# Performance work log

Hardware: AMD Instinct MI355X
Metric: run time of the kernel (lower is better)

The kernel has to match this reference:

```python
import jax, jax.numpy as jnp
import numpy as np

B, S, D = 2, 2048, 1024
N_HEADS = 16
PAT_HEADS = N_HEADS // 4          # MultiheadAttention num_heads = 4
HEAD_DIM = D // PAT_HEADS         # 256
SPARSITY_RATIO = 0.1
MEMORY_PRESSURE = 0.5
NEG_INF = -1e9


def setup_inputs() -> dict:
    key = jax.random.key(0)
    ks = jax.random.split(key, 16)
    sd = 1.0 / np.sqrt(D)
    sh = 1.0 / np.sqrt(D // 4)
    inp = {
        "q": jax.random.normal(ks[0], (B, S, D), jnp.float32),
        "k": jax.random.normal(ks[1], (B, S, D), jnp.float32),
        "v": jax.random.normal(ks[2], (B, S, D), jnp.float32),
        # sparsity predictor: Linear(D, D//4) -> ReLU -> Linear(D//4, 1) -> Sigmoid
        "w1": jax.random.uniform(ks[3], (D, D // 4), jnp.float32, -sd, sd),
        "b1": jax.random.uniform(ks[4], (D // 4,), jnp.float32, -sd, sd),
        "w2": jax.random.uniform(ks[5], (D // 4, 1), jnp.float32, -sh, sh),
        "b2": jax.random.uniform(ks[6], (1,), jnp.float32, -sh, sh),
        # MultiheadAttention in_proj (split) + out_proj, stored [in, out]
        "wq": jax.random.uniform(ks[7], (D, D), jnp.float32, -sd, sd),
        "bq": jnp.zeros((D,), jnp.float32),
        "wk": jax.random.uniform(ks[8], (D, D), jnp.float32, -sd, sd),
        "bk": jnp.zeros((D,), jnp.float32),
        "wv": jax.random.uniform(ks[9], (D, D), jnp.float32, -sd, sd),
        "bv": jnp.zeros((D,), jnp.float32),
        "wo": jax.random.uniform(ks[10], (D, D), jnp.float32, -sd, sd),
        "bo": jnp.zeros((D,), jnp.float32),
    }
    return inp


def reference(q, k, v, w1, b1, w2, b2, wq, bq, wk, bk, wv, bv, wo, bo):
    # learned importance scores -> boolean mask of active tokens
    h = jax.nn.relu(q @ w1 + b1)                       # [B,S,D//4]
    scores = jax.nn.sigmoid(h @ w2 + b2)[..., 0]       # [B,S]
    threshold = SPARSITY_RATIO * (1.0 + MEMORY_PRESSURE)
    mask = scores > threshold                          # [B,S] bool

    # original module flattens all active tokens across batch into ONE
    # sequence and runs MHA over that subset; we express the identical math
    # with a fixed-shape masked attention over the flattened [B*S] tokens.
    N = B * S
    mf = mask.reshape(N)                               # [N]
    qf = q.reshape(N, D)
    kf = k.reshape(N, D)
    vf = v.reshape(N, D)

    qp = (qf @ wq + bq).reshape(N, PAT_HEADS, HEAD_DIM)
    kp = (kf @ wk + bk).reshape(N, PAT_HEADS, HEAD_DIM)
    vp = (vf @ wv + bv).reshape(N, PAT_HEADS, HEAD_DIM)

    scale = 1.0 / np.sqrt(HEAD_DIM)
    logits = jnp.einsum("nhd,mhd->hnm", qp * scale, kp)   # [H,N,N]
    logits = jnp.where(mf[None, None, :], logits, NEG_INF)  # only active keys
    attn = jax.nn.softmax(logits, axis=-1)
    ctx = jnp.einsum("hnm,mhd->nhd", attn, vp).reshape(N, D)
    out = ctx @ wo + bo                                 # [N,D]

    # scatter back: inactive query positions stay zero
    out = jnp.where(mf[:, None], out, 0.0)
    return out.reshape(B, S, D)
```

## Files before the change

kernel.cpp:

```cpp
#include <hip/hip_runtime.h>
#include <hip/hip_bf16.h>
#include <math.h>

typedef __bf16 bf16x8 __attribute__((ext_vector_type(8)));
typedef __bf16 bf16x4 __attribute__((ext_vector_type(4)));
typedef float  f32x4  __attribute__((ext_vector_type(4)));
typedef short  s16x8  __attribute__((ext_vector_type(8)));

#define N_TOK  4096
#define DMODEL 1024
#define NHEAD  4
#define DHEAD  256

__device__ __forceinline__ f32x4 mfma16x16(bf16x8 a, bf16x8 b, f32x4 c) {
    return __builtin_amdgcn_mfma_f32_16x16x32_bf16(a, b, c, 0, 0, 0);
}

__device__ __forceinline__ void gload_lds16(const void* gsrc, void* ldst) {
    __builtin_amdgcn_global_load_lds(
        (const __attribute__((address_space(1))) void*)gsrc,
        (__attribute__((address_space(3))) void*)ldst, 16, 0, 0);
}

#define G_LDT 72

template<typename OutT, bool AF32>
__global__ __launch_bounds__(256, 2)
void gemm_mixed(const void* __restrict__ Av, int lda,
                const float* __restrict__ B, int ldb,
                const float* __restrict__ bias,
                OutT* __restrict__ C, int ldc,
                float scale, int relu, const float* __restrict__ rowmask)
{
    __shared__ __align__(16) short As[64 * G_LDT];
    __shared__ __align__(16) short Bs[128 * G_LDT];
    const int tid  = threadIdx.x;
    const int lane = tid & 63;
    const int wv   = tid >> 6;
    const int c16  = lane & 15;
    const int quad = lane >> 4;
    const int m0 = blockIdx.x * 64;
    const int n0 = blockIdx.y * 128;

    f32x4 acc[4][2];
    #pragma unroll
    for (int i = 0; i < 4; ++i)
        #pragma unroll
        for (int j = 0; j < 2; ++j)
            acc[i][j] = (f32x4){0.f, 0.f, 0.f, 0.f};

    const int bn = tid & 127;
    const int bh = tid >> 7;

    for (int k0 = 0; k0 < 1024; k0 += 64) {
        if (AF32) {
            const float* A = (const float*)Av;
            #pragma unroll
            for (int r = 0; r < 4; ++r) {
                int i = tid + r * 256;
                int m = i >> 4, c = i & 15;
                f32x4 t = *(const f32x4*)(A + (size_t)(m0 + m) * lda + k0 + c * 4);
                bf16x4 b;
                #pragma unroll
                for (int j = 0; j < 4; ++j) b[j] = (__bf16)t[j];
                *(bf16x4*)(&As[m * G_LDT + c * 4]) = b;
            }
        } else {
            const __bf16* A = (const __bf16*)Av;
            #pragma unroll
            for (int r = 0; r < 2; ++r) {
                int i = tid + r * 256;
                int m = i >> 3, c = i & 7;
                *(s16x8*)(&As[m * G_LDT + c * 8]) =
                    *(const s16x8*)(A + (size_t)(m0 + m) * lda + k0 + c * 8);
            }
        }
        {
            const float* bp = B + (size_t)(k0 + bh * 32) * ldb + n0 + bn;
            #pragma unroll
            for (int g = 0; g < 4; ++g) {
                bf16x8 t;
                #pragma unroll
                for (int j = 0; j < 8; ++j) t[j] = (__bf16)bp[(size_t)(g * 8 + j) * ldb];
                *(bf16x8*)(&Bs[bn * G_LDT + bh * 32 + g * 8]) = t;
            }
        }
        __syncthreads();
        #pragma unroll
        for (int ks = 0; ks < 2; ++ks) {
            bf16x8 af[4], bfr[2];
            #pragma unroll
            for (int t = 0; t < 4; ++t)
                af[t] = *(const bf16x8*)(&As[(t * 16 + c16) * G_LDT + ks * 32 + quad * 8]);
            #pragma unroll
            for (int t = 0; t < 2; ++t)
                bfr[t] = *(const bf16x8*)(&Bs[(wv * 32 + t * 16 + c16) * G_LDT + ks * 32 + quad * 8]);
            #pragma unroll
            for (int tm = 0; tm < 4; ++tm)
                #pragma unroll
                for (int tn = 0; tn < 2; ++tn)
                    acc[tm][tn] = mfma16x16(af[tm], bfr[tn], acc[tm][tn]);
        }
        __syncthreads();
    }

    #pragma unroll
    for (int tm = 0; tm < 4; ++tm) {
        #pragma unroll
        for (int r = 0; r < 4; ++r) {
            int row = m0 + tm * 16 + quad * 4 + r;
            float mk = rowmask ? rowmask[row] : 1.0f;
            #pragma unroll
            for (int tn = 0; tn < 2; ++tn) {
                int col = n0 + wv * 32 + tn * 16 + c16;
                float val = (acc[tm][tn][r] + bias[col]) * scale;
                if (relu) val = fmaxf(val, 0.0f);
                val *= mk;
                C[(size_t)row * ldc + col] = (OutT)val;
            }
        }
    }
}

__global__ void score_mask_kernel(const __bf16* __restrict__ h,
                                  const float* __restrict__ w2,
                                  const float* __restrict__ b2,
                                  float* __restrict__ maskf)
{
    int lane = threadIdx.x & 63;
    int tok  = blockIdx.x * 4 + (threadIdx.x >> 6);
    const __bf16* hr = h + (size_t)tok * 256;
    float s = 0.f;
    #pragma unroll
    for (int j = 0; j < 4; ++j) {
        int c = j * 64 + lane;
        s += (float)hr[c] * w2[c];
    }
    #pragma unroll
    for (int o = 1; o < 64; o <<= 1) s += __shfl_xor(s, o);
    if (lane == 0) {
        float x = s + b2[0];
        maskf[tok] = (x > -1.7346010553881064f) ? 1.0f : 0.0f;
    }
}

__global__ __launch_bounds__(256)
void transpose_kernel(const __bf16* __restrict__ in, __bf16* __restrict__ out)
{
    __shared__ __align__(16) short tile[64 * 72];
    const int tid = threadIdx.x;
    const int t0 = blockIdx.x * 64;
    const int c0 = blockIdx.y * 64;
    #pragma unroll
    for (int it = 0; it < 2; ++it) {
        int i = tid + it * 256;
        int tok = i >> 3, ch = i & 7;
        s16x8 v = *(const s16x8*)((const short*)in + (size_t)(t0 + tok) * DMODEL + c0 + ch * 8);
        #pragma unroll
        for (int j = 0; j < 8; ++j)
            tile[(ch * 8 + j) * 72 + tok] = v[j];
    }
    __syncthreads();
    #pragma unroll
    for (int it = 0; it < 2; ++it) {
        int i = tid + it * 256;
        int col = i >> 3, och = i & 7;
        s16x8 v = *(const s16x8*)(&tile[col * 72 + och * 8]);
        *(s16x8*)((short*)out + (size_t)(c0 + col) * N_TOK + t0 + och * 8) = v;
    }
}

template<bool SPLIT>
__global__ __launch_bounds__(256, 2)
void attn_kernel(const __bf16* __restrict__ qp, const __bf16* __restrict__ kp,
                 const __bf16* __restrict__ vpT, const float* __restrict__ maskf,
                 __bf16* __restrict__ O0, __bf16* __restrict__ O1,
                 float* __restrict__ lbuf)
{
    __shared__ __align__(16) short Ks[64 * 256];
    __shared__ __align__(16) short Vs[256 * 64];
    __shared__ __align__(16) short PsA[4 * 16 * 64];

    const int tid  = threadIdx.x;
    const int lane = tid & 63;
    const int wv   = tid >> 6;
    const int c16  = lane & 15;
    const int quad = lane >> 4;
    const int swz  = c16 & 7;
    const int head = blockIdx.y;
    const int ksp  = SPLIT ? blockIdx.z : 0;
    const int kbase = ksp * (SPLIT ? 2048 : 0);
    const int kend  = kbase + (SPLIT ? 2048 : 4096);
    const int q0   = blockIdx.x * 64 + wv * 16;
    short* Ps = PsA + wv * 16 * 64;
    __bf16* Ob = (SPLIT && ksp == 1) ? O1 : O0;

    bf16x8 qf[8];
    #pragma unroll
    for (int c = 0; c < 8; ++c)
        qf[c] = *(const bf16x8*)(qp + (size_t)(q0 + c16) * DMODEL + head * DHEAD + c * 32 + quad * 8);

    f32x4 o[16];
    #pragma unroll
    for (int t = 0; t < 16; ++t) o[t] = (f32x4){0.f, 0.f, 0.f, 0.f};
    float psum[4] = {0.f, 0.f, 0.f, 0.f};

    const int kRow0 = wv * 16 + (lane >> 5);
    const int kCh   = lane & 31;
    const int vRow0 = wv * 64 + (lane >> 3);
    const int vCh   = (lane & 7) ^ ((lane >> 3) & 7);

    #pragma unroll 1
    for (int n0 = kbase; n0 < kend; n0 += 64) {
        #pragma unroll
        for (int g = 0; g < 8; ++g) {
            int key = kRow0 + g * 2;
            int c   = kCh ^ (key & 7);
            const char* src = (const char*)(kp + (size_t)(n0 + key) * DMODEL + head * DHEAD) + c * 16;
            gload_lds16(src, (char*)Ks + (wv * 16 + g * 2) * 512);
        }
        #pragma unroll
        for (int g = 0; g < 8; ++g) {
            int row = vRow0 + g * 8;
            const char* src = (const char*)(vpT + (size_t)(head * DHEAD + row) * N_TOK + n0) + vCh * 16;
            gload_lds16(src, (char*)Vs + (wv * 64 + g * 8) * 128);
        }
        __syncthreads();

        f32x4 s[4];
        #pragma unroll
        for (int kt = 0; kt < 4; ++kt) s[kt] = (f32x4){0.f, 0.f, 0.f, 0.f};
        __builtin_amdgcn_s_setprio(1);
        #pragma unroll
        for (int c = 0; c < 8; ++c)
            #pragma unroll
            for (int kt = 0; kt < 4; ++kt) {
                bf16x8 bfr = *(const bf16x8*)(&Ks[(kt * 16 + c16) * 256 + (((c * 4 + quad) ^ swz) << 3)]);
                s[kt] = mfma16x16(qf[c], bfr, s[kt]);
            }
        __builtin_amdgcn_s_setprio(0);

        #pragma unroll
        for (int kt = 0; kt < 4; ++kt) {
            float biasv = (maskf[n0 + kt * 16 + c16] - 1.0f) * 1e9f;
            #pragma unroll
            for (int r = 0; r < 4; ++r) {
                float p = __expf(s[kt][r] + biasv);
                psum[r] += p;
                int qrow = quad * 4 + r;
                int ch = (kt * 2 + (c16 >> 3)) ^ (qrow & 7);
                *(__bf16*)&Ps[qrow * 64 + ch * 8 + swz] = (__bf16)p;
            }
        }

        __builtin_amdgcn_s_waitcnt(0xc07f);

        __builtin_amdgcn_s_setprio(1);
        #pragma unroll
        for (int kstep = 0; kstep < 2; ++kstep) {
            bf16x8 pf = *(const bf16x8*)(&Ps[c16 * 64 + (((kstep * 4 + quad) ^ swz) << 3)]);
            #pragma unroll
            for (int t = 0; t < 16; ++t) {
                bf16x8 vf = *(const bf16x8*)(&Vs[(t * 16 + c16) * 64 + (((kstep * 4 + quad) ^ swz) << 3)]);
                o[t] = mfma16x16(pf, vf, o[t]);
            }
        }
        __builtin_amdgcn_s_setprio(0);
        __syncthreads();
    }

    float inv[4];
    #pragma unroll
    for (int r = 0; r < 4; ++r) {
        float t = psum[r];
        t += __shfl_xor(t, 1);
        t += __shfl_xor(t, 2);
        t += __shfl_xor(t, 4);
        t += __shfl_xor(t, 8);
        if (SPLIT && c16 == 0)
            lbuf[(size_t)(ksp * NHEAD + head) * N_TOK + q0 + quad * 4 + r] = t;
        inv[r] = 1.0f / t;
    }
    #pragma unroll
    for (int t = 0; t < 16; ++t)
        #pragma unroll
        for (int r = 0; r < 4; ++r) {
            float val = o[t][r] * inv[r];
            Ob[(size_t)(q0 + quad * 4 + r) * DMODEL + head * DHEAD + t * 16 + c16] = (__bf16)val;
        }
}

__global__ void combine_kernel(const __bf16* __restrict__ O0,
                               const __bf16* __restrict__ O1,
                               const float* __restrict__ lbuf,
                               __bf16* __restrict__ out)
{
    int idx  = blockIdx.x * 256 + threadIdx.x;
    int tok  = idx >> 7;
    int g    = idx & 127;
    int head = g >> 5;
    float a = lbuf[(size_t)head * N_TOK + tok];
    float b = lbuf[(size_t)(NHEAD + head) * N_TOK + tok];
    float w0 = a / (a + b);
    float w1 = 1.0f - w0;
    size_t off = (size_t)tok * DMODEL + g * 8;
    bf16x8 x = *(const bf16x8*)(O0 + off);
    bf16x8 y = *(const bf16x8*)(O1 + off);
    bf16x8 z;
    #pragma unroll
    for (int j = 0; j < 8; ++j) z[j] = (__bf16)(w0 * (float)x[j] + w1 * (float)y[j]);
    *(bf16x8*)(out + off) = z;
}

extern "C" void kernel_launch(void* const* d_in, const int* in_sizes, int n_in,
                              void* d_out, int out_size, void* d_ws, size_t ws_size,
                              hipStream_t stream)
{
    (void)in_sizes; (void)n_in; (void)out_size;
    const float* q  = (const float*)d_in[0];
    const float* k  = (const float*)d_in[1];
    const float* v  = (const float*)d_in[2];
    const float* w1 = (const float*)d_in[3];
    const float* b1 = (const float*)d_in[4];
    const float* w2 = (const float*)d_in[5];
    const float* b2 = (const float*)d_in[6];
    const float* wq = (const float*)d_in[7];
    const float* bq = (const float*)d_in[8];
    const float* wk = (const float*)d_in[9];
    const float* bk = (const float*)d_in[10];
    const float* wvw = (const float*)d_in[11];
    const float* bv = (const float*)d_in[12];
    const float* wo = (const float*)d_in[13];
    const float* bo = (const float*)d_in[14];

    if (ws_size < 35667968u) return;

    char* ws = (char*)d_ws;
    float*  maskf = (float*)ws;
    __bf16* hbuf  = (__bf16*)(ws + 16384);
    __bf16* qp    = (__bf16*)(ws + 16384 + 2097152);
    __bf16* kpb   = qp  + 4194304;
    __bf16* vpb   = kpb + 4194304;
    __bf16* ctx   = vpb + 4194304;
    __bf16* O1    = (__bf16*)(ws + 35667968u);
    float*  lbuf  = (float*)(ws + 35667968u + 8388608u);
    const bool split = ws_size >= 35667968u + 8388608u + 131072u;

    __bf16* vpT = (__bf16*)d_out;

    gemm_mixed<__bf16, true><<<dim3(64, 2), 256, 0, stream>>>(q, 1024, w1, 256, b1, hbuf, 256, 1.0f, 1, nullptr);
    score_mask_kernel<<<1024, 256, 0, stream>>>(hbuf, w2, b2, maskf);
    gemm_mixed<__bf16, true><<<dim3(64, 8), 256, 0, stream>>>(q, 1024, wq, 1024, bq, qp, 1024, 0.0625f, 0, nullptr);
    gemm_mixed<__bf16, true><<<dim3(64, 8), 256, 0, stream>>>(k, 1024, wk, 1024, bk, kpb, 1024, 1.0f, 0, nullptr);
    gemm_mixed<__bf16, true><<<dim3(64, 8), 256, 0, stream>>>(v, 1024, wvw, 1024, bv, vpb, 1024, 1.0f, 0, nullptr);
    transpose_kernel<<<dim3(64, 16), 256, 0, stream>>>(vpb, vpT);

    if (split) {
        attn_kernel<true><<<dim3(64, 4, 2), 256, 0, stream>>>(qp, kpb, vpT, maskf, ctx, O1, lbuf);
        combine_kernel<<<2048, 256, 0, stream>>>(ctx, O1, lbuf, ctx);
    } else {
        attn_kernel<false><<<dim3(64, 4, 1), 256, 0, stream>>>(qp, kpb, vpT, maskf, ctx, nullptr, nullptr);
    }

    gemm_mixed<float, false><<<dim3(64, 8), 256, 0, stream>>>(ctx, 1024, wo, 1024, bo, (float*)d_out, 1024, 1.0f, 0, maskf);
}
```

Baseline: 359.0 us.

## Pre-transpose weights to bf16 and compute V projection directly transposed

Adds a weight transpose-and-convert kernel so every GEMM reads a K-contiguous bf16 B operand instead of doing strided per-element fp32 loads of the weights. The GEMM is reworked to a 128x64 tile with an XOR-swizzled LDS layout, uses direct global-to-LDS loads for bf16 operands, and raises wave priority around the MFMA section. The V projection is computed as wvT·vᵀ with a per-row bias, which writes V already transposed and removes the separate activation transpose kernel. It costs five extra transpose launches per call and reuses the output and hbuf buffers as scratch for the transposed weights.

```diff
diff --git a/kernel.cpp b/kernel.cpp
--- a/kernel.cpp
+++ b/kernel.cpp
@@ -22,25 +22,53 @@
         (__attribute__((address_space(3))) void*)ldst, 16, 0, 0);
 }
 
-#define G_LDT 72
-
-template<typename OutT, bool AF32>
+__global__ __launch_bounds__(256)
+void transposew_kernel(const float* __restrict__ in, __bf16* __restrict__ out,
+                       int R, int C)
+{
+    __shared__ __align__(16) __bf16 tile[64 * 72];
+    const int tid = threadIdx.x;
+    const int r0 = blockIdx.x * 64;
+    const int c0 = blockIdx.y * 64;
+    #pragma unroll
+    for (int it = 0; it < 4; ++it) {
+        int i = tid + it * 256;
+        int row = i >> 4, c4 = i & 15;
+        f32x4 v = *(const f32x4*)(in + (size_t)(r0 + row) * C + c0 + c4 * 4);
+        #pragma unroll
+        for (int j = 0; j < 4; ++j)
+            tile[(c4 * 4 + j) * 72 + row] = (__bf16)v[j];
+    }
+    __syncthreads();
+    #pragma unroll
+    for (int it = 0; it < 2; ++it) {
+        int i = tid + it * 256;
+        int col = i >> 3, ch = i & 7;
+        s16x8 v = *(const s16x8*)(&tile[col * 72 + ch * 8]);
+        *(s16x8*)((short*)out + (size_t)(c0 + col) * R + r0 + ch * 8) = v;
+    }
+}
+
+template<typename OutT, bool AF32, bool BF32, bool BIASROW>
 __global__ __launch_bounds__(256, 2)
-void gemm_mixed(const void* __restrict__ Av, int lda,
-                const float* __restrict__ B, int ldb,
-                const float* __restrict__ bias,
-                OutT* __restrict__ C, int ldc,
-                float scale, int relu, const float* __restrict__ rowmask)
-{
-    __shared__ __align__(16) short As[64 * G_LDT];
-    __shared__ __align__(16) short Bs[128 * G_LDT];
+void gemm_bt(const void* __restrict__ Av, int lda,
+             const void* __restrict__ Bv, int ldb,
+             const float* __restrict__ bias,
+             OutT* __restrict__ C, int ldc,
+             float scale, int relu, const float* __restrict__ rowmask, int K)
+{
+    __shared__ __align__(16) short As[128 * 64];
+    __shared__ __align__(16) short Bs[64 * 64];
     const int tid  = threadIdx.x;
     const int lane = tid & 63;
     const int wv   = tid >> 6;
     const int c16  = lane & 15;
     const int quad = lane >> 4;
-    const int m0 = blockIdx.x * 64;
-    const int n0 = blockIdx.y * 128;
+    const int swz  = c16 & 7;
+    const int wr   = wv >> 1;
+    const int wc   = wv & 1;
+    const int m0 = blockIdx.x * 128;
+    const int n0 = blockIdx.y * 64;
 
     f32x4 acc[4][2];
     #pragma unroll
@@ -49,71 +77,92 @@
         for (int j = 0; j < 2; ++j)
             acc[i][j] = (f32x4){0.f, 0.f, 0.f, 0.f};
 
-    const int bn = tid & 127;
-    const int bh = tid >> 7;
-
-    for (int k0 = 0; k0 < 1024; k0 += 64) {
+    const int sRow = lane >> 3;
+    const int sCh  = (lane & 7) ^ (sRow & 7);
+
+    #pragma unroll 1
+    for (int k0 = 0; k0 < K; k0 += 64) {
         if (AF32) {
             const float* A = (const float*)Av;
             #pragma unroll
             for (int r = 0; r < 4; ++r) {
-                int i = tid + r * 256;
-                int m = i >> 4, c = i & 15;
-                f32x4 t = *(const f32x4*)(A + (size_t)(m0 + m) * lda + k0 + c * 4);
-                bf16x4 b;
+                int idx = tid + r * 256;
+                int row = idx >> 3, ch = idx & 7;
+                const float* ap = A + (size_t)(m0 + row) * lda + k0 + ch * 8;
+                f32x4 t0 = *(const f32x4*)ap;
+                f32x4 t1 = *(const f32x4*)(ap + 4);
+                bf16x8 b;
                 #pragma unroll
-                for (int j = 0; j < 4; ++j) b[j] = (__bf16)t[j];
-                *(bf16x4*)(&As[m * G_LDT + c * 4]) = b;
+                for (int j = 0; j < 4; ++j) { b[j] = (__bf16)t0[j]; b[j + 4] = (__bf16)t1[j]; }
+                *(bf16x8*)((char*)As + row * 128 + ((ch ^ (row & 7)) * 16)) = b;
             }
         } else {
             const __bf16* A = (const __bf16*)Av;
             #pragma unroll
+            for (int g = 0; g < 4; ++g) {
+                int row = 32 * wv + 8 * g + sRow;
+                const char* src = (const char*)(A + (size_t)(m0 + row) * lda + k0) + sCh * 16;
+                gload_lds16(src, (char*)As + (32 * wv + 8 * g) * 128);
+            }
+        }
+        if (BF32) {
+            const float* B = (const float*)Bv;
+            #pragma unroll
             for (int r = 0; r < 2; ++r) {
-                int i = tid + r * 256;
-                int m = i >> 3, c = i & 7;
-                *(s16x8*)(&As[m * G_LDT + c * 8]) =
-                    *(const s16x8*)(A + (size_t)(m0 + m) * lda + k0 + c * 8);
-            }
-        }
-        {
-            const float* bp = B + (size_t)(k0 + bh * 32) * ldb + n0 + bn;
-            #pragma unroll
-            for (int g = 0; g < 4; ++g) {
-                bf16x8 t;
+                int idx = tid + r * 256;
+                int row = idx >> 3, ch = idx & 7;
+                const float* bp = B + (size_t)(n0 + row) * ldb + k0 + ch * 8;
+                f32x4 t0 = *(const f32x4*)bp;
+                f32x4 t1 = *(const f32x4*)(bp + 4);
+                bf16x8 b;
                 #pragma unroll
-                for (int j = 0; j < 8; ++j) t[j] = (__bf16)bp[(size_t)(g * 8 + j) * ldb];
-                *(bf16x8*)(&Bs[bn * G_LDT + bh * 32 + g * 8]) = t;
+                for (int j = 0; j < 4; ++j) { b[j] = (__bf16)t0[j]; b[j + 4] = (__bf16)t1[j]; }
+                *(bf16x8*)((char*)Bs + row * 128 + ((ch ^ (row & 7)) * 16)) = b;
+            }
+        } else {
+            const __bf16* B = (const __bf16*)Bv;
+            #pragma unroll
+            for (int g = 0; g < 2; ++g) {
+                int row = 16 * wv + 8 * g + sRow;
+                const char* src = (const char*)(B + (size_t)(n0 + row) * ldb + k0) + sCh * 16;
+                gload_lds16(src, (char*)Bs + (16 * wv + 8 * g) * 128);
             }
         }
         __syncthreads();
+
+        __builtin_amdgcn_s_setprio(1);
         #pragma unroll
         for (int ks = 0; ks < 2; ++ks) {
             bf16x8 af[4], bfr[2];
+            int slot = ((ks * 4 + quad) ^ swz) * 16;
             #pragma unroll
             for (int t = 0; t < 4; ++t)
-                af[t] = *(const bf16x8*)(&As[(t * 16 + c16) * G_LDT + ks * 32 + quad * 8]);
+                af[t] = *(const bf16x8*)((char*)As + (wr * 64 + t * 16 + c16) * 128 + slot);
             #pragma unroll
             for (int t = 0; t < 2; ++t)
-                bfr[t] = *(const bf16x8*)(&Bs[(wv * 32 + t * 16 + c16) * G_LDT + ks * 32 + quad * 8]);
+                bfr[t] = *(const bf16x8*)((char*)Bs + (wc * 32 + t * 16 + c16) * 128 + slot);
             #pragma unroll
             for (int tm = 0; tm < 4; ++tm)
                 #pragma unroll
                 for (int tn = 0; tn < 2; ++tn)
                     acc[tm][tn] = mfma16x16(af[tm], bfr[tn], acc[tm][tn]);
         }
+        __builtin_amdgcn_s_setprio(0);
         __syncthreads();
     }
 
     #pragma unroll
     for (int tm = 0; tm < 4; ++tm) {
         #pragma unroll
-        for (int r = 0; r < 4; ++r) {
-            int row = m0 + tm * 16 + quad * 4 + r;
+        for (int rr = 0; rr < 4; ++rr) {
+            int row = m0 + wr * 64 + tm * 16 + quad * 4 + rr;
             float mk = rowmask ? rowmask[row] : 1.0f;
+            float rb = BIASROW ? bias[row] : 0.0f;
             #pragma unroll
             for (int tn = 0; tn < 2; ++tn) {
-                int col = n0 + wv * 32 + tn * 16 + c16;
-                float val = (acc[tm][tn][r] + bias[col]) * scale;
+                int col = n0 + wc * 32 + tn * 16 + c16;
+                float b = BIASROW ? rb : bias[col];
+                float val = (acc[tm][tn][rr] + b) * scale;
                 if (relu) val = fmaxf(val, 0.0f);
                 val *= mk;
                 C[(size_t)row * ldc + col] = (OutT)val;
@@ -141,32 +190,6 @@
     if (lane == 0) {
         float x = s + b2[0];
         maskf[tok] = (x > -1.7346010553881064f) ? 1.0f : 0.0f;
-    }
-}
-
-__global__ __launch_bounds__(256)
-void transpose_kernel(const __bf16* __restrict__ in, __bf16* __restrict__ out)
-{
-    __shared__ __align__(16) short tile[64 * 72];
-    const int tid = threadIdx.x;
-    const int t0 = blockIdx.x * 64;
-    const int c0 = blockIdx.y * 64;
-    #pragma unroll
-    for (int it = 0; it < 2; ++it) {
-        int i = tid + it * 256;
-        int tok = i >> 3, ch = i & 7;
-        s16x8 v = *(const s16x8*)((const short*)in + (size_t)(t0 + tok) * DMODEL + c0 + ch * 8);
-        #pragma unroll
-        for (int j = 0; j < 8; ++j)
-            tile[(ch * 8 + j) * 72 + tok] = v[j];
-    }
-    __syncthreads();
-    #pragma unroll
-    for (int it = 0; it < 2; ++it) {
-        int i = tid + it * 256;
-        int col = i >> 3, och = i & 7;
-        s16x8 v = *(const s16x8*)(&tile[col * 72 + och * 8]);
-        *(s16x8*)((short*)out + (size_t)(c0 + col) * N_TOK + t0 + och * 8) = v;
     }
 }
 
@@ -340,20 +363,34 @@
     __bf16* hbuf  = (__bf16*)(ws + 16384);
     __bf16* qp    = (__bf16*)(ws + 16384 + 2097152);
     __bf16* kpb   = qp  + 4194304;
-    __bf16* vpb   = kpb + 4194304;
-    __bf16* ctx   = vpb + 4194304;
+    __bf16* vpT   = kpb + 4194304;
+    __bf16* ctx   = vpT + 4194304;
     __bf16* O1    = (__bf16*)(ws + 35667968u);
     float*  lbuf  = (float*)(ws + 35667968u + 8388608u);
     const bool split = ws_size >= 35667968u + 8388608u + 131072u;
 
-    __bf16* vpT = (__bf16*)d_out;
-
-    gemm_mixed<__bf16, true><<<dim3(64, 2), 256, 0, stream>>>(q, 1024, w1, 256, b1, hbuf, 256, 1.0f, 1, nullptr);
+    __bf16* wqT = (__bf16*)d_out;
+    __bf16* wkT = wqT + 1048576;
+    __bf16* wvT = wkT + 1048576;
+    __bf16* w1T = wvT + 1048576;
+    __bf16* woT = hbuf;
+
+    transposew_kernel<<<dim3(16, 4), 256, 0, stream>>>(w1, w1T, 1024, 256);
+    gemm_bt<__bf16, true, false, false><<<dim3(32, 4), 256, 0, stream>>>(
+        q, 1024, w1T, 1024, b1, hbuf, 256, 1.0f, 1, nullptr, 1024);
     score_mask_kernel<<<1024, 256, 0, stream>>>(hbuf, w2, b2, maskf);
-    gemm_mixed<__bf16, true><<<dim3(64, 8), 256, 0, stream>>>(q, 1024, wq, 1024, bq, qp, 1024, 0.0625f, 0, nullptr);
-    gemm_mixed<__bf16, true><<<dim3(64, 8), 256, 0, stream>>>(k, 1024, wk, 1024, bk, kpb, 1024, 1.0f, 0, nullptr);
-    gemm_mixed<__bf16, true><<<dim3(64, 8), 256, 0, stream>>>(v, 1024, wvw, 1024, bv, vpb, 1024, 1.0f, 0, nullptr);
-    transpose_kernel<<<dim3(64, 16), 256, 0, stream>>>(vpb, vpT);
+
+    transposew_kernel<<<dim3(16, 16), 256, 0, stream>>>(wq, wqT, 1024, 1024);
+    transposew_kernel<<<dim3(16, 16), 256, 0, stream>>>(wk, wkT, 1024, 1024);
+    transposew_kernel<<<dim3(16, 16), 256, 0, stream>>>(wvw, wvT, 1024, 1024);
+    transposew_kernel<<<dim3(16, 16), 256, 0, stream>>>(wo, woT, 1024, 1024);
+
+    gemm_bt<__bf16, true, false, false><<<dim3(32, 16), 256, 0, stream>>>(
+        q, 1024, wqT, 1024, bq, qp, 1024, 0.0625f, 0, nullptr, 1024);
+    gemm_bt<__bf16, true, false, false><<<dim3(32, 16), 256, 0, stream>>>(
+        k, 1024, wkT, 1024, bk, kpb, 1024, 1.0f, 0, nullptr, 1024);
+    gemm_bt<__bf16, false, true, true><<<dim3(8, 64), 256, 0, stream>>>(
+        wvT, 1024, v, 1024, bv, vpT, 4096, 1.0f, 0, nullptr, 1024);
 
     if (split) {
         attn_kernel<true><<<dim3(64, 4, 2), 256, 0, stream>>>(qp, kpb, vpT, maskf, ctx, O1, lbuf);
@@ -362,5 +399,6 @@
         attn_kernel<false><<<dim3(64, 4, 1), 256, 0, stream>>>(qp, kpb, vpT, maskf, ctx, nullptr, nullptr);
     }
 
-    gemm_mixed<float, false><<<dim3(64, 8), 256, 0, stream>>>(ctx, 1024, wo, 1024, bo, (float*)d_out, 1024, 1.0f, 0, maskf);
-}
+    gemm_bt<float, false, false, false><<<dim3(32, 16), 256, 0, stream>>>(
+        ctx, 1024, woT, 1024, bo, (float*)d_out, 1024, 1.0f, 0, maskf, 1024);
+}
```

After: 406.0 us. 1.13x slower.
